# Kernel tuning notes

Hardware: AMD Instinct MI355X
Metric: run time of the kernel (lower is better)

The kernel has to match this reference:

```python
import jax, jax.numpy as jnp
import numpy as np

N = 16384   # total nodes in batch
E = 65536   # edges
B = 512     # sessions
L = 32      # nodes per session
H = 64      # hidden_size
HEADS = 16  # GAT heads (layer 1)
K = 3       # interests
V = 32000   # n_node (item vocab)
NEG = 0.2   # leaky relu slope


def _u(k, shape, stdv):
    return jax.random.uniform(k, shape, jnp.float32, -stdv, stdv)


def setup_inputs():
    key = jax.random.key(0)
    ks = jax.random.split(key, 24)
    s = 1.0 / np.sqrt(H)  # reset_parameters: uniform(-stdv, stdv)
    D = K * H
    return {
        "x": jax.random.randint(ks[0], (N,), 0, V),
        "edge_index": jax.random.randint(ks[1], (2, E), 0, N),
        "batch": jnp.repeat(jnp.arange(B, dtype=jnp.int32), L),
        "embedding": _u(ks[2], (V, H), s),
        "w_interest": _u(ks[3], (H, K), s),
        "gat1_W": _u(ks[4], (K, H, HEADS * H), s),
        "gat1_as": _u(ks[5], (K, HEADS, H), s),
        "gat1_ad": _u(ks[6], (K, HEADS, H), s),
        "gat1_b": _u(ks[7], (K, HEADS * H), s),
        "gat2_W": _u(ks[8], (K, HEADS * H, H), s),
        "gat2_as": _u(ks[9], (K, 1, H), s),
        "gat2_ad": _u(ks[10], (K, 1, H), s),
        "gat2_b": _u(ks[11], (K, H), s),
        "W1_w": _u(ks[12], (D, D), s), "W1_b": _u(ks[13], (D,), s),
        "W2_w": _u(ks[14], (D, D), s), "W2_b": _u(ks[15], (D,), s),
        "q_w": _u(ks[16], (D, 1), s), "q_b": _u(ks[17], (1,), s),
        "W3_w": _u(ks[18], (2 * D, D), s), "W3_b": _u(ks[19], (D,), s),
    }


def _gat(h_in, W, b, a_s, a_d, src, dst, valid, heads, out):
    """PyG GATConv: per-head linear, edge softmax over dest, self-loops for all nodes."""
    n = h_in.shape[0]
    h = (h_in @ W).reshape(n, heads, out)          # [n, heads, out]
    asrc = (h * a_s[None]).sum(-1)                 # [n, heads]
    adst = (h * a_d[None]).sum(-1)
    loop = jnp.arange(n)
    fs = jnp.concatenate([src, loop])              # edges + self-loops
    fd = jnp.concatenate([dst, loop])
    v = jnp.concatenate([valid, jnp.ones((n,), bool)])
    logits = jax.nn.leaky_relu(asrc[fs] + adst[fd], NEG)   # [E+n, heads]
    logits = jnp.where(v[:, None], logits, -1e9)
    m = jax.ops.segment_max(logits, fd, num_segments=n)
    p = jnp.exp(logits - m[fd]) * v[:, None]
    denom = jax.ops.segment_sum(p, fd, num_segments=n)     # [n, heads]
    num = jax.ops.segment_sum(p[:, :, None] * h[fs], fd, num_segments=n)
    return (num / denom[:, :, None]).reshape(n, heads * out) + b


def _model(x, edge_index, batch, embedding, w_interest,
           gat1_W, gat1_as, gat1_ad, gat1_b,
           gat2_W, gat2_as, gat2_ad, gat2_b,
           W1_w, W1_b, W2_w, W2_b, q_w, q_b, W3_w, W3_b):
    e = embedding[x]                                # [N, H]
    g = jax.nn.softmax((e @ w_interest) / 0.1, axis=-1)   # [N, K]
    mask = g > (1.0 / K)                            # interest_mask
    src, dst = edge_index[0], edge_index[1]
    hiddens = []
    for i in range(K):                              # fixed small interest loop
        xi = g[:, i:i + 1] * e                      # einsum('ik,il->ikl')[:, i]
        valid = mask[src, i] & mask[dst, i]         # subgraph edge mask
        h1 = jax.nn.relu(_gat(xi, gat1_W[i], gat1_b[i], gat1_as[i], gat1_ad[i],
                              src, dst, valid, HEADS, H))
        h2 = _gat(h1, gat2_W[i], gat2_b[i], gat2_as[i], gat2_ad[i],
                  src, dst, valid, 1, H)
        hiddens.append(h2)
    sess = jnp.concatenate(hiddens, axis=1)         # [N, K*H]
    # Embedding2Score
    last_idx = jax.ops.segment_max(jnp.arange(N), batch, num_segments=B)
    v_n = sess[last_idx]                            # [B, K*H]  last node per session
    q1 = v_n[batch] @ W1_w + W1_b                   # v_n repeated per node
    q2 = sess @ W2_w + W2_b
    alpha = jax.nn.sigmoid(q1 + q2) @ q_w + q_b     # [N, 1]
    s_g = jax.ops.segment_sum(alpha * sess, batch, num_segments=B)
    s_h = jnp.concatenate([v_n, s_g], axis=1) @ W3_w + W3_b   # [B, K*H]
    s_h = s_h.reshape(B * K, H)                     # multi-interest split
    z = s_h @ embedding.T                           # [B*K, V]
    return z.reshape(B, K, V).max(axis=1)           # [B, V]


def reference(x, edge_index, batch, embedding, w_interest,
              gat1_W, gat1_as, gat1_ad, gat1_b,
              gat2_W, gat2_as, gat2_ad, gat2_b,
              W1_w, W1_b, W2_w, W2_b, q_w, q_b, W3_w, W3_b):
    return _model(x, edge_index, batch, embedding, w_interest,
                  gat1_W, gat1_as, gat1_ad, gat1_b,
                  gat2_W, gat2_as, gat2_ad, gat2_b,
                  W1_w, W1_b, W2_w, W2_b, q_w, q_b, W3_w, W3_b)
```

## Files before the change

kernel.cpp:

```cpp
#include <hip/hip_runtime.h>
#include <math.h>

#define NN 16384
#define EE 65536
#define BB 512
#define VV 32000

typedef unsigned short us_t;
typedef unsigned int u32_t;
typedef __attribute__((ext_vector_type(4))) float f32x4;
typedef __attribute__((ext_vector_type(8))) short bf16x8;
typedef __attribute__((ext_vector_type(4))) unsigned int u32x4;

__device__ __forceinline__ float bf2f(unsigned int u) {
  return __uint_as_float((u & 0xffffu) << 16);
}
__device__ __forceinline__ unsigned short f2bf(float f) {
  unsigned int x = __float_as_uint(f);
  unsigned int r = (x + 0x7fffu + ((x >> 16) & 1u)) >> 16;
  return (unsigned short)r;
}
__device__ __forceinline__ bf16x8 ntld(const us_t* p) {
  return __builtin_nontemporal_load((const bf16x8*)p);
}
__device__ __forceinline__ void ntst(us_t* p, u32_t a, u32_t b, u32_t c, u32_t d) {
  u32x4 v = {a, b, c, d};
  __builtin_nontemporal_store(v, (u32x4*)p);
}
__device__ __forceinline__ float wsum(float v) {
#pragma unroll
  for (int o = 32; o; o >>= 1) v += __shfl_xor(v, o, 64);
  return v;
}
__device__ __forceinline__ float redu16(float v) {
  v += __shfl_xor(v, 1, 64);
  v += __shfl_xor(v, 2, 64);
  v += __shfl_xor(v, 4, 64);
  v += __shfl_xor(v, 8, 64);
  return v;
}
__device__ __forceinline__ float lrelu(float x) { return x > 0.f ? x : 0.2f * x; }

__global__ void k_detect(const void* emb, int* flag) {
  if (threadIdx.x == 0 && blockIdx.x == 0) {
    const us_t* u = (const us_t*)emb;
    int ok = 1;
    for (int i = 0; i < 128; i++) {
      float v = bf2f((unsigned int)u[i]);
      if (!(fabsf(v) <= 0.13f)) { ok = 0; break; }
    }
    *flag = ok;
  }
}

struct PrepArgs {
  const void* src[17];
  void* dst[17];
  int n[17];
  int kind[17];
  int start[18];
};

__global__ void k_prep(PrepArgs pa, const int* __restrict__ flag) {
  int blk = blockIdx.x;
  int s = 0;
  while (s < 16 && blk >= pa.start[s + 1]) s++;
  int i = (blk - pa.start[s]) * 256 + threadIdx.x;
  if (i >= pa.n[s]) return;
  float v = (*flag) ? bf2f((unsigned int)((const us_t*)pa.src[s])[i])
                    : ((const float*)pa.src[s])[i];
  int kind = pa.kind[s];
  if (kind == 0) {
    ((float*)pa.dst[s])[i] = v;
  } else if (kind == 1) {
    ((us_t*)pa.dst[s])[i] = f2bf(v);
  } else if (kind == 2) {
    int ii = i >> 16, r = i & 65535, k = r >> 10, col = r & 1023;
    ((us_t*)pa.dst[s])[(ii << 16) + col * 64 + k] = f2bf(v);
  } else if (kind == 3) {
    int ii = i >> 16, r = i & 65535, k = r >> 6, col = r & 63;
    ((us_t*)pa.dst[s])[(ii << 16) + col * 1024 + k] = f2bf(v);
  } else {
    int k = i / 192, col = i % 192;
    ((us_t*)pa.dst[s])[col * 192 + k] = f2bf(v);
  }
}

__global__ void k_prepWa(const void* __restrict__ g1Wraw,
                         const float* __restrict__ g1as, const float* __restrict__ g1ad,
                         const int* __restrict__ flag, us_t* __restrict__ Waspack) {
  int gid = blockIdx.x * 256 + threadIdx.x;
  if (gid >= 96 * 64) return;
  int c = gid >> 6, k = gid & 63;
  int i = c >> 5, sd = (c >> 4) & 1, h = c & 15;
  const float* av = (sd ? g1ad : g1as) + i * 1024 + h * 64;
  size_t base = (size_t)i * 65536 + (size_t)k * 1024 + h * 64;
  int isbf = *flag;
  float s = 0.f;
  for (int d = 0; d < 64; d++) {
    float wv = isbf ? bf2f((unsigned int)((const us_t*)g1Wraw)[base + d])
                    : ((const float*)g1Wraw)[base + d];
    s += wv * av[d];
  }
  Waspack[c * 64 + k] = f2bf(s);
}

__global__ void k_embed(const int* __restrict__ x, const void* __restrict__ embr,
                        const void* __restrict__ wintr, const int* __restrict__ flag,
                        us_t* __restrict__ e_bf, float* __restrict__ g) {
  int gid = blockIdx.x * blockDim.x + threadIdx.x;
  int n = gid >> 6, lane = gid & 63;
  if (n >= NN) return;
  int isbf = *flag;
  size_t ei = (size_t)x[n] * 64 + lane;
  float v = isbf ? bf2f((unsigned int)((const us_t*)embr)[ei]) : ((const float*)embr)[ei];
  e_bf[(size_t)n * 64 + lane] = f2bf(v);
  float w0, w1, w2;
  if (isbf) {
    const us_t* w = (const us_t*)wintr;
    w0 = bf2f(w[lane * 3 + 0]); w1 = bf2f(w[lane * 3 + 1]); w2 = bf2f(w[lane * 3 + 2]);
  } else {
    const float* w = (const float*)wintr;
    w0 = w[lane * 3 + 0]; w1 = w[lane * 3 + 1]; w2 = w[lane * 3 + 2];
  }
  float t0 = wsum(v * w0), t1 = wsum(v * w1), t2 = wsum(v * w2);
  if (lane == 0) {
    float l0 = t0 / 0.1f, l1 = t1 / 0.1f, l2 = t2 / 0.1f;
    float m = fmaxf(l0, fmaxf(l1, l2));
    float p0 = __expf(l0 - m), p1 = __expf(l1 - m), p2 = __expf(l2 - m);
    float inv = 1.0f / (p0 + p1 + p2);
    g[n * 4 + 0] = p0 * inv; g[n * 4 + 1] = p1 * inv;
    g[n * 4 + 2] = p2 * inv; g[n * 4 + 3] = 0.f;
  }
}

__global__ void k_countv(const int* __restrict__ ei, const float* __restrict__ g,
                         int* __restrict__ countsv) {
  int e = blockIdx.x * 256 + threadIdx.x;
  if (e >= EE) return;
  int s = ei[e], d = ei[EE + e];
  const float thr = 1.0f / 3.0f;
#pragma unroll
  for (int i = 0; i < 3; i++) {
    if (g[s * 4 + i] > thr && g[d * 4 + i] > thr)
      atomicAdd(&countsv[i * NN + d], 1);
  }
}

__global__ void k_scanv(const int* __restrict__ counts, int* __restrict__ offsets) {
  __shared__ int part[256];
  __shared__ int excl[257];
  int t = threadIdx.x;
  int base = t * 192;
  int s = 0;
  for (int j = 0; j < 192; j++) s += counts[base + j];
  part[t] = s;
  __syncthreads();
  if (t == 0) {
    int run = 0;
    for (int j = 0; j < 256; j++) { excl[j] = run; run += part[j]; }
    excl[256] = run;
  }
  __syncthreads();
  int run = excl[t];
  for (int j = 0; j < 192; j++) { offsets[base + j] = run; run += counts[base + j]; }
  if (t == 255) offsets[3 * NN] = excl[256];
}

__global__ void k_fillv(const int* __restrict__ ei, const float* __restrict__ g,
                        const float* __restrict__ eatt,
                        const int* __restrict__ offsetsv, int* __restrict__ fillposv,
                        int2* __restrict__ edgesC, float* __restrict__ easrcP) {
  int e = blockIdx.x * 256 + threadIdx.x;
  if (e >= EE) return;
  int s = ei[e], d = ei[EE + e];
  const float thr = 1.0f / 3.0f;
#pragma unroll
  for (int i = 0; i < 3; i++) {
    float gs = g[s * 4 + i];
    if (gs > thr && g[d * 4 + i] > thr) {
      int pos = offsetsv[i * NN + d] + atomicAdd(&fillposv[i * NN + d], 1);
      edgesC[pos] = make_int2(s, __float_as_int(gs));
      const float* er = &eatt[(size_t)s * 96 + i * 32];
      float* op = &easrcP[(size_t)pos * 16];
#pragma unroll
      for (int h = 0; h < 16; h++) op[h] = gs * er[h];
    }
  }
}

__global__ __launch_bounds__(256) void k_easrc(
    const us_t* __restrict__ e_bf, const us_t* __restrict__ Waspack,
    float* __restrict__ eatt) {
  __shared__ char As[8192];
  int t = threadIdx.x;
  int row0 = blockIdx.x * 64;
  for (int id = t; id < 512; id += 256) {
    int r = id >> 3, c = id & 7;
    uint4 v = *(const uint4*)&e_bf[(size_t)(row0 + r) * 64 + c * 8];
    *(uint4*)(As + r * 128 + ((c ^ (r & 7)) << 4)) = v;
  }
  __syncthreads();
  int wv = t >> 6, L = t & 63, li = L & 15, lq = L >> 4;
#pragma unroll
  for (int ct = 0; ct < 6; ct++) {
    f32x4 acc = {0.f, 0.f, 0.f, 0.f};
#pragma unroll
    for (int ks = 0; ks < 2; ks++) {
      int row = wv * 16 + li;
      bf16x8 af = *(const bf16x8*)(As + row * 128 + (((ks * 4 + lq) ^ (row & 7)) << 4));
      bf16x8 bfr = *(const bf16x8*)(Waspack + (size_t)(ct * 16 + li) * 64 + ks * 32 + lq * 8);
      acc = __builtin_amdgcn_mfma_f32_16x16x32_bf16(af, bfr, acc, 0, 0, 0);
    }
#pragma unroll
    for (int r = 0; r < 4; r++) {
      int row = row0 + wv * 16 + lq * 4 + r;
      eatt[(size_t)row * 96 + ct * 16 + li] = acc[r];
    }
  }
}

__global__ __launch_bounds__(256) void k_phaseA(
    const us_t* __restrict__ e_bf, const float* __restrict__ g,
    const float* __restrict__ eatt,
    const int* __restrict__ offsetsv, const int2* __restrict__ edgesC,
    const float* __restrict__ easrcP, us_t* __restrict__ xagg) {
  int t = threadIdx.x;
  int intr = blockIdx.y;
  int wv = t >> 6, L = t & 63;
  int n = blockIdx.x * 4 + wv;
  int h = L >> 2;
  int doff = (L & 3) * 16;
  float gn = g[n * 4 + intr];
  float ad = gn * eatt[(size_t)n * 96 + intr * 32 + 16 + h];
  float m = lrelu(gn * eatt[(size_t)n * 96 + intr * 32 + h] + ad);
  float den = 1.f;
  float acc[16];
  {
    const uint4* ep = (const uint4*)&e_bf[(size_t)n * 64 + doff];
    uint4 a = ep[0], b = ep[1];
    acc[0] = gn * bf2f(a.x);  acc[1] = gn * bf2f(a.x >> 16);
    acc[2] = gn * bf2f(a.y);  acc[3] = gn * bf2f(a.y >> 16);
    acc[4] = gn * bf2f(a.z);  acc[5] = gn * bf2f(a.z >> 16);
    acc[6] = gn * bf2f(a.w);  acc[7] = gn * bf2f(a.w >> 16);
    acc[8] = gn * bf2f(b.x);  acc[9] = gn * bf2f(b.x >> 16);
    acc[10] = gn * bf2f(b.y); acc[11] = gn * bf2f(b.y >> 16);
    acc[12] = gn * bf2f(b.z); acc[13] = gn * bf2f(b.z >> 16);
    acc[14] = gn * bf2f(b.w); acc[15] = gn * bf2f(b.w >> 16);
  }
  int beg = offsetsv[intr * NN + n], end = offsetsv[intr * NN + n + 1];
  for (int j = beg; j < end; j++) {
    int2 sg = edgesC[j];
    int s = sg.x;
    float gs = __int_as_float(sg.y);
    float l = lrelu(easrcP[(size_t)j * 16 + h] + ad);
    float p = __expf(l - m);
    den += p;
    float pg = p * gs;
    const uint4* ep = (const uint4*)&e_bf[(size_t)s * 64 + doff];
    uint4 a = ep[0], b = ep[1];
    acc[0] += pg * bf2f(a.x);  acc[1] += pg * bf2f(a.x >> 16);
    acc[2] += pg * bf2f(a.y);  acc[3] += pg * bf2f(a.y >> 16);
    acc[4] += pg * bf2f(a.z);  acc[5] += pg * bf2f(a.z >> 16);
    acc[6] += pg * bf2f(a.w);  acc[7] += pg * bf2f(a.w >> 16);
    acc[8] += pg * bf2f(b.x);  acc[9] += pg * bf2f(b.x >> 16);
    acc[10] += pg * bf2f(b.y); acc[11] += pg * bf2f(b.y >> 16);
    acc[12] += pg * bf2f(b.z); acc[13] += pg * bf2f(b.z >> 16);
    acc[14] += pg * bf2f(b.w); acc[15] += pg * bf2f(b.w >> 16);
  }
  float inv = 1.f / den;
  u32_t w[8];
#pragma unroll
  for (int kk = 0; kk < 8; kk++) {
    w[kk] = (u32_t)f2bf(acc[2 * kk] * inv) | ((u32_t)f2bf(acc[2 * kk + 1] * inv) << 16);
  }
  us_t* op = &xagg[(((size_t)intr * 16 + h) * NN + n) * 64 + doff];
  ntst(op, w[0], w[1], w[2], w[3]);
  ntst(op + 8, w[4], w[5], w[6], w[7]);
}

__global__ __launch_bounds__(256) void k_tgemm(
    const us_t* __restrict__ xagg, const us_t* __restrict__ g1Wt,
    const float* __restrict__ b1all, us_t* __restrict__ Tbuf) {
  __shared__ char As[8192];
  __shared__ char Cs[8192];
  int t = threadIdx.x;
  int n0 = blockIdx.x * 64;
  int h = blockIdx.y;
  int intr = blockIdx.z;
  const us_t* xa = xagg + (((size_t)intr * 16 + h) * NN + n0) * 64;
  const us_t* W = g1Wt + (size_t)intr * 65536 + (size_t)(h * 64) * 64;
  const float* b1 = b1all + intr * 1024 + h * 64;
  for (int id = t; id < 512; id += 256) {
    int r = id >> 3, c = id & 7;
    bf16x8 v = ntld(&xa[(size_t)r * 64 + c * 8]);
    *(bf16x8*)(As + r * 128 + ((c ^ (r & 7)) << 4)) = v;
  }
  __syncthreads();
  int wv = t >> 6, L = t & 63, li = L & 15, lq = L >> 4;
  f32x4 acc[4];
#pragma unroll
  for (int ct = 0; ct < 4; ct++) acc[ct] = {0.f, 0.f, 0.f, 0.f};
#pragma unroll
  for (int ks = 0; ks < 2; ks++) {
    int row = wv * 16 + li;
    bf16x8 af = *(const bf16x8*)(As + row * 128 + (((ks * 4 + lq) ^ (row & 7)) << 4));
#pragma unroll
    for (int ct = 0; ct < 4; ct++) {
      bf16x8 bfr = *(const bf16x8*)&W[(size_t)(ct * 16 + li) * 64 + ks * 32 + lq * 8];
      acc[ct] = __builtin_amdgcn_mfma_f32_16x16x32_bf16(af, bfr, acc[ct], 0, 0, 0);
    }
  }
#pragma unroll
  for (int ct = 0; ct < 4; ct++) {
    float bv = b1[ct * 16 + li];
#pragma unroll
    for (int r = 0; r < 4; r++) {
      int row = wv * 16 + lq * 4 + r;
      int byte = (ct * 16 + li) * 2;
      float tv = fmaxf(acc[ct][r] + bv, 0.f);
      *(us_t*)(Cs + row * 128 + (((byte >> 4) ^ (row & 7)) << 4) + (byte & 15)) = f2bf(tv);
    }
  }
  __syncthreads();
  us_t* tb = Tbuf + (((size_t)intr * 16 + h) * NN + n0) * 64;
  for (int id = t; id < 512; id += 256) {
    int r = id >> 3, c = id & 7;
    bf16x8 v = *(const bf16x8*)(Cs + r * 128 + ((c ^ (r & 7)) << 4));
    __builtin_nontemporal_store(v, (bf16x8*)&tb[(size_t)r * 64 + c * 8]);
  }
}

__global__ __launch_bounds__(256) void k_h2gemm(
    const us_t* __restrict__ Tbuf, const us_t* __restrict__ g2Wt,
    const float* __restrict__ g2as, const float* __restrict__ g2ad,
    float* __restrict__ h2pre_a, float* __restrict__ a2s, float* __restrict__ a2d) {
  __shared__ uint4 AsU[1024];
  __shared__ uint4 BsU[1024];
  char* As = (char*)AsU;
  char* Bs = (char*)BsU;
  int t = threadIdx.x;
  int intr = blockIdx.y;
  int row0 = blockIdx.x * 64;
  const us_t* Wt = g2Wt + (size_t)intr * 65536;
  const float* a_s = g2as + intr * 64;
  const float* a_d = g2ad + intr * 64;
  float* h2pre = h2pre_a + (size_t)intr * NN * 64;
  int wv = t >> 6, lane = t & 63, li = lane & 15, lq = lane >> 4;
  f32x4 acc[4];
#pragma unroll
  for (int sub = 0; sub < 4; sub++) acc[sub] = {0.f, 0.f, 0.f, 0.f};
  for (int kb = 0; kb < 8; kb++) {
    __syncthreads();
    for (int id = t; id < 1024; id += 256) {
      int r = id >> 4, c = id & 15;
      int k = kb * 128 + c * 8;
      int h = k >> 6, d = k & 63;
      bf16x8 v = ntld(&Tbuf[(((size_t)intr * 16 + h) * NN + row0 + r) * 64 + d]);
      *(bf16x8*)(As + r * 256 + ((c ^ (r & 15)) << 4)) = v;
      uint4 w = *(const uint4*)&Wt[(size_t)r * 1024 + kb * 128 + c * 8];
      *(uint4*)(Bs + r * 256 + ((c ^ (r & 15)) << 4)) = w;
    }
    __syncthreads();
#pragma unroll
    for (int ks = 0; ks < 4; ks++) {
      int r = wv * 16 + li;
      bf16x8 af = *(const bf16x8*)(As + r * 256 + ((((ks << 2) | lq) ^ (r & 15)) << 4));
#pragma unroll
      for (int sub = 0; sub < 4; sub++) {
        int vr = sub * 16 + li;
        bf16x8 bf_ = *(const bf16x8*)(Bs + vr * 256 + ((((ks << 2) | lq) ^ (vr & 15)) << 4));
        acc[sub] = __builtin_amdgcn_mfma_f32_16x16x32_bf16(af, bf_, acc[sub], 0, 0, 0);
      }
    }
  }
  float asv[4], adv[4];
#pragma unroll
  for (int sub = 0; sub < 4; sub++) {
    asv[sub] = a_s[sub * 16 + li];
    adv[sub] = a_d[sub * 16 + li];
  }
#pragma unroll
  for (int rr = 0; rr < 4; rr++) {
    int n = row0 + wv * 16 + lq * 4 + rr;
    float s = 0.f, d = 0.f;
#pragma unroll
    for (int sub = 0; sub < 4; sub++) {
      float hv = acc[sub][rr];
      h2pre[(size_t)n * 64 + sub * 16 + li] = hv;
      s += hv * asv[sub];
      d += hv * adv[sub];
    }
    s = redu16(s); d = redu16(d);
    if (li == 0) {
      a2s[(size_t)intr * NN + n] = s;
      a2d[(size_t)intr * NN + n] = d;
    }
  }
}

__global__ void k_gat2_agg(const float* __restrict__ h2pre_a,
                           const float* __restrict__ a2s_a, const float* __restrict__ a2d_a,
                           const float* __restrict__ b2all,
                           const int* __restrict__ offsetsv,
                           const int2* __restrict__ edgesC, float* __restrict__ sess) {
  int intr = blockIdx.y;
  int gid = blockIdx.x * blockDim.x + threadIdx.x;
  int n = gid >> 6, lane = gid & 63;
  if (n >= NN) return;
  const float* h2pre = h2pre_a + (size_t)intr * NN * 64;
  const float* a2s = a2s_a + (size_t)intr * NN;
  const float* a2d = a2d_a + (size_t)intr * NN;
  const float* b2 = b2all + intr * 64;
  float ad = a2d[n];
  float m = lrelu(a2s[n] + ad);
  float den = 1.f;
  float acc = h2pre[(size_t)n * 64 + lane];
  int beg = offsetsv[intr * NN + n], end = offsetsv[intr * NN + n + 1];
  for (int j = beg; j < end; j++) {
    int s = edgesC[j].x;
    float l = lrelu(a2s[s] + ad);
    float p = __expf(l - m);
    den += p;
    acc += p * h2pre[(size_t)s * 64 + lane];
  }
  sess[(size_t)n * 192 + intr * 64 + lane] = acc / den + b2[lane];
}

__global__ __launch_bounds__(192) void k_vq1(
    const float* __restrict__ sess,
    const float* __restrict__ W1w, const float* __restrict__ W1b,
    float* __restrict__ vn, float* __restrict__ vq1) {
  __shared__ float row[192];
  int b = blockIdx.x, j = threadIdx.x;
  int li = b * 32 + 31;
  float v = sess[(size_t)li * 192 + j];
  row[j] = v;
  vn[b * 192 + j] = v;
  __syncthreads();
  float acc = W1b[j];
  for (int k = 0; k < 192; k++) acc += row[k] * W1w[k * 192 + j];
  vq1[b * 192 + j] = acc;
}

__global__ __launch_bounds__(256) void k_alpha_sg_mfma(
    const float* __restrict__ sess, const float* __restrict__ vq1,
    const us_t* __restrict__ W2T, const float* __restrict__ W2b,
    const float* __restrict__ qw, const float* __restrict__ qb,
    float* __restrict__ sg) {
  __shared__ char As[64 * 512];
  __shared__ float vq_l[2 * 192];
  __shared__ float w2b_l[192], qw_l[192];
  __shared__ float sg_l[2 * 192];
  int t = threadIdx.x;
  int n0 = blockIdx.x * 64;
  if (t < 192) { w2b_l[t] = W2b[t]; qw_l[t] = qw[t]; }
  for (int id = t; id < 384; id += 256) {
    sg_l[id] = 0.f;
    vq_l[id] = vq1[(size_t)(blockIdx.x * 2) * 192 + id];
  }
  for (int id = t; id < 1536; id += 256) {
    int r = id / 24, c = id % 24;
    const float* p = &sess[(size_t)(n0 + r) * 192 + c * 8];
    float4 f0 = *(const float4*)p;
    float4 f1 = *(const float4*)(p + 4);
    u32_t w0 = (u32_t)f2bf(f0.x) | ((u32_t)f2bf(f0.y) << 16);
    u32_t w1 = (u32_t)f2bf(f0.z) | ((u32_t)f2bf(f0.w) << 16);
    u32_t w2 = (u32_t)f2bf(f1.x) | ((u32_t)f2bf(f1.y) << 16);
    u32_t w3 = (u32_t)f2bf(f1.z) | ((u32_t)f2bf(f1.w) << 16);
    *(uint4*)(As + r * 512 + ((c ^ (r & 7)) << 4)) = make_uint4(w0, w1, w2, w3);
  }
  __syncthreads();
  int wv = t >> 6, lane = t & 63, li = lane & 15, lq = lane >> 4;
  int sl = wv >> 1;
  f32x4 acc[12];
#pragma unroll
  for (int sub = 0; sub < 12; sub++) acc[sub] = {0.f, 0.f, 0.f, 0.f};
#pragma unroll
  for (int ks = 0; ks < 6; ks++) {
    int r = wv * 16 + li;
    bf16x8 af = *(const bf16x8*)(As + r * 512 + (((ks * 4 + lq) ^ (r & 7)) << 4));
#pragma unroll
    for (int sub = 0; sub < 12; sub++) {
      bf16x8 bfr = *(const bf16x8*)&W2T[(size_t)(sub * 16 + li) * 192 + ks * 32 + lq * 8];
      acc[sub] = __builtin_amdgcn_mfma_f32_16x16x32_bf16(af, bfr, acc[sub], 0, 0, 0);
    }
  }
  float qbv = qb[0];
  float s_part[12];
#pragma unroll
  for (int sub = 0; sub < 12; sub++) s_part[sub] = 0.f;
#pragma unroll
  for (int rr = 0; rr < 4; rr++) {
    int n = n0 + wv * 16 + lq * 4 + rr;
    float ap = 0.f;
    float sv[12];
#pragma unroll
    for (int sub = 0; sub < 12; sub++) {
      int col = sub * 16 + li;
      float q = vq_l[sl * 192 + col] + acc[sub][rr] + w2b_l[col];
      float sgm = 1.f / (1.f + __expf(-q));
      ap += sgm * qw_l[col];
      sv[sub] = sess[(size_t)n * 192 + col];
    }
    ap = redu16(ap);
    float alpha = ap + qbv;
#pragma unroll
    for (int sub = 0; sub < 12; sub++) s_part[sub] += alpha * sv[sub];
  }
#pragma unroll
  for (int sub = 0; sub < 12; sub++) {
    float v = s_part[sub];
    v += __shfl_xor(v, 16, 64);
    v += __shfl_xor(v, 32, 64);
    if (lq == 0) atomicAdd(&sg_l[sl * 192 + sub * 16 + li], v);
  }
  __syncthreads();
  for (int id = t; id < 384; id += 256)
    sg[(size_t)(blockIdx.x * 2) * 192 + id] = sg_l[id];
}

__global__ __launch_bounds__(192) void k_sh(
    const float* __restrict__ vn, const float* __restrict__ sg,
    const float* __restrict__ W3w, const float* __restrict__ W3b,
    float* __restrict__ sh) {
  __shared__ float row[384];
  int b = blockIdx.x, j = threadIdx.x;
  row[j] = vn[b * 192 + j];
  row[192 + j] = sg[b * 192 + j];
  __syncthreads();
  float acc = W3b[j];
  for (int k = 0; k < 384; k++) acc += row[k] * W3w[k * 192 + j];
  sh[b * 192 + j] = acc;
}

__global__ __launch_bounds__(256) void k_final_mfma(
    const float* __restrict__ sh, const us_t* __restrict__ emb_bf,
    void* __restrict__ out, const int* __restrict__ flag) {
  __shared__ uint4 AsU[384];
  __shared__ uint4 BsU[2048];
  char* As = (char*)AsU;
  char* Bs = (char*)BsU;
  int t = threadIdx.x;
  int v0 = blockIdx.x * 256, b0 = blockIdx.y * 16;
  for (int id = t; id < 384; id += 256) {
    int i2 = id >> 7, rem = id & 127, r = rem >> 3, c = rem & 7;
    const float* p = &sh[(size_t)(b0 + r) * 192 + i2 * 64 + c * 8];
    float4 f0 = *(const float4*)p;
    float4 f1 = *(const float4*)(p + 4);
    u32_t w0 = (u32_t)f2bf(f0.x) | ((u32_t)f2bf(f0.y) << 16);
    u32_t w1 = (u32_t)f2bf(f0.z) | ((u32_t)f2bf(f0.w) << 16);
    u32_t w2 = (u32_t)f2bf(f1.x) | ((u32_t)f2bf(f1.y) << 16);
    u32_t w3 = (u32_t)f2bf(f1.z) | ((u32_t)f2bf(f1.w) << 16);
    *(uint4*)(As + i2 * 2048 + r * 128 + ((c ^ (r & 7)) << 4)) = make_uint4(w0, w1, w2, w3);
  }
  for (int id = t; id < 2048; id += 256) {
    int vr = id >> 3, c = id & 7;
    uint4 v = *(const uint4*)&emb_bf[(size_t)(v0 + vr) * 64 + c * 8];
    *(uint4*)(Bs + vr * 128 + ((c ^ (vr & 7)) << 4)) = v;
  }
  __syncthreads();
  int wv = t >> 6, lane = t & 63, li = lane & 15, lq = lane >> 4;
  int cb = wv * 64;
  int isbf = *flag;
  f32x4 acc[3][4];
#pragma unroll
  for (int i = 0; i < 3; i++)
#pragma unroll
    for (int sub = 0; sub < 4; sub++) acc[i][sub] = {0.f, 0.f, 0.f, 0.f};
#pragma unroll
  for (int ks = 0; ks < 2; ks++) {
    bf16x8 bfr[4];
#pragma unroll
    for (int sub = 0; sub < 4; sub++) {
      int vr = cb + sub * 16 + li;
      bfr[sub] = *(const bf16x8*)(Bs + vr * 128 + ((((ks << 2) | lq) ^ (vr & 7)) << 4));
    }
#pragma unroll
    for (int i = 0; i < 3; i++) {
      bf16x8 af = *(const bf16x8*)(As + i * 2048 + li * 128 + ((((ks << 2) | lq) ^ (li & 7)) << 4));
#pragma unroll
      for (int sub = 0; sub < 4; sub++)
        acc[i][sub] = __builtin_amdgcn_mfma_f32_16x16x32_bf16(af, bfr[sub], acc[i][sub], 0, 0, 0);
    }
  }
#pragma unroll
  for (int sub = 0; sub < 4; sub++) {
    int col = v0 + cb + sub * 16 + li;
#pragma unroll
    for (int rr = 0; rr < 4; rr++) {
      float o = fmaxf(fmaxf(acc[0][sub][rr], acc[1][sub][rr]), acc[2][sub][rr]);
      int b = b0 + lq * 4 + rr;
      if (isbf) ((us_t*)out)[(size_t)b * VV + col] = f2bf(o);
      else ((float*)out)[(size_t)b * VV + col] = o;
    }
  }
}

extern "C" void kernel_launch(void* const* d_in, const int* in_sizes, int n_in,
                              void* d_out, int out_size, void* d_ws, size_t ws_size,
                              hipStream_t stream) {
  if (n_in < 21) return;
  const int* x = (const int*)d_in[0];
  const int* ei = (const int*)d_in[1];

  char* ws = (char*)d_ws;
  size_t off = 0;
  auto A = [&](size_t bytes) -> char* {
    char* p = ws + off;
    off += (bytes + 255) & ~(size_t)255;
    return p;
  };
  int* flag = (int*)A(4);
  us_t* emb_bf = (us_t*)A((size_t)VV * 64 * 2);
  us_t* e_bf = (us_t*)A((size_t)NN * 64 * 2);
  us_t* g1Wt = (us_t*)A((size_t)3 * 65536 * 2);
  us_t* g2Wt = (us_t*)A((size_t)3 * 65536 * 2);
  us_t* W2T = (us_t*)A((size_t)36864 * 2);
  us_t* Waspack = (us_t*)A((size_t)96 * 64 * 2);
  float* eatt = (float*)A((size_t)NN * 96 * 4);
  float* c_g1as = (float*)A(3072 * 4);
  float* c_g1ad = (float*)A(3072 * 4);
  float* c_g1b = (float*)A(3072 * 4);
  float* c_g2as = (float*)A(192 * 4);
  float* c_g2ad = (float*)A(192 * 4);
  float* c_g2b = (float*)A(192 * 4);
  float* c_W1w = (float*)A(36864 * 4);
  float* c_W1b = (float*)A(192 * 4);
  float* c_W2b = (float*)A(192 * 4);
  float* c_qw = (float*)A(192 * 4);
  float* c_qb = (float*)A(4);
  float* c_W3w = (float*)A(73728 * 4);
  float* c_W3b = (float*)A(192 * 4);
  float* g_buf = (float*)A((size_t)NN * 4 * 4);
  us_t* xagg = (us_t*)A((size_t)3 * NN * 1024 * 2);
  us_t* Tbuf = (us_t*)A((size_t)3 * NN * 1024 * 2);
  float* h2pre = (float*)A((size_t)3 * NN * 64 * 4);
  float* a2s = (float*)A((size_t)3 * NN * 4);
  float* a2d = (float*)A((size_t)3 * NN * 4);
  float* sess = (float*)A((size_t)NN * 192 * 4);
  float* vq1 = (float*)A((size_t)BB * 192 * 4);
  float* sg = (float*)A((size_t)BB * 192 * 4);
  float* vn = (float*)A((size_t)BB * 192 * 4);
  float* shb = (float*)A((size_t)BB * 192 * 4);
  int* countsv = (int*)A((size_t)3 * NN * 4);
  int* offsetsv = (int*)A((size_t)(3 * NN + 1) * 4);
  int* fillposv = (int*)A((size_t)3 * NN * 4);
  int2* edgesC = (int2*)A((size_t)3 * EE * 8);
  float* easrcP = (float*)A((size_t)3 * EE * 16 * 4);
  if (off > ws_size) return;

  hipMemsetAsync(countsv, 0, 3 * NN * 4, stream);
  hipMemsetAsync(fillposv, 0, 3 * NN * 4, stream);

  k_detect<<<1, 64, 0, stream>>>(d_in[3], flag);

  PrepArgs pa;
  int nb = 0, idx = 0;
  auto SEC = [&](const void* s, void* d, int n, int kind) {
    pa.src[idx] = s; pa.dst[idx] = d; pa.n[idx] = n; pa.kind[idx] = kind;
    pa.start[idx] = nb; nb += (n + 255) / 256; idx++;
  };
  SEC(d_in[3], emb_bf, VV * 64, 1);
  SEC(d_in[5], g1Wt, 196608, 2);
  SEC(d_in[9], g2Wt, 196608, 3);
  SEC(d_in[15], W2T, 36864, 4);
  SEC(d_in[6], c_g1as, 3072, 0);
  SEC(d_in[7], c_g1ad, 3072, 0);
  SEC(d_in[8], c_g1b, 3072, 0);
  SEC(d_in[10], c_g2as, 192, 0);
  SEC(d_in[11], c_g2ad, 192, 0);
  SEC(d_in[12], c_g2b, 192, 0);
  SEC(d_in[13], c_W1w, 36864, 0);
  SEC(d_in[14], c_W1b, 192, 0);
  SEC(d_in[16], c_W2b, 192, 0);
  SEC(d_in[17], c_qw, 192, 0);
  SEC(d_in[18], c_qb, 1, 0);
  SEC(d_in[19], c_W3w, 73728, 0);
  SEC(d_in[20], c_W3b, 192, 0);
  pa.start[17] = nb;
  k_prep<<<nb, 256, 0, stream>>>(pa, flag);
  k_prepWa<<<24, 256, 0, stream>>>(d_in[5], c_g1as, c_g1ad, flag, Waspack);

  k_embed<<<NN * 64 / 256, 256, 0, stream>>>(x, d_in[3], d_in[4], flag, e_bf, g_buf);
  k_easrc<<<NN / 64, 256, 0, stream>>>(e_bf, Waspack, eatt);
  k_countv<<<EE / 256, 256, 0, stream>>>(ei, g_buf, countsv);
  k_scanv<<<1, 256, 0, stream>>>(countsv, offsetsv);
  k_fillv<<<EE / 256, 256, 0, stream>>>(ei, g_buf, eatt, offsetsv, fillposv,
                                        edgesC, easrcP);

  k_phaseA<<<dim3(NN / 4, 3), 256, 0, stream>>>(
      e_bf, g_buf, eatt, offsetsv, edgesC, easrcP, xagg);
  k_tgemm<<<dim3(NN / 64, 16, 3), 256, 0, stream>>>(xagg, g1Wt, c_g1b, Tbuf);
  k_h2gemm<<<dim3(NN / 64, 3), 256, 0, stream>>>(
      Tbuf, g2Wt, c_g2as, c_g2ad, h2pre, a2s, a2d);
  k_gat2_agg<<<dim3(NN * 64 / 256, 3), 256, 0, stream>>>(
      h2pre, a2s, a2d, c_g2b, offsetsv, edgesC, sess);

  k_vq1<<<BB, 192, 0, stream>>>(sess, c_W1w, c_W1b, vn, vq1);
  k_alpha_sg_mfma<<<NN / 64, 256, 0, stream>>>(sess, vq1, W2T, c_W2b, c_qw, c_qb, sg);
  k_sh<<<BB, 192, 0, stream>>>(vn, sg, c_W3w, c_W3b, shb);
  k_final_mfma<<<dim3(VV / 256, BB / 16), 256, 0, stream>>>(shb, emb_bf, d_out, flag);
}
```

Measured before the change: 294.6 us.

## Fuse GAT layer-1 head GEMM into layer-2 GEMM, dropping Tbuf round trip

Removes the separate per-head transform kernel and computes relu(xagg·W1+b1) per head tile inside the layer-2 GEMM, keeping the intermediate in LDS. This eliminates writing and re-reading a large bf16 intermediate buffer in global memory and one kernel launch. In exchange the fused kernel has fewer blocks, more LDS per block, and re-reads the layer-1 weights per block from cache.

```diff
diff --git a/kernel.cpp b/kernel.cpp
--- a/kernel.cpp
+++ b/kernel.cpp
@@ -279,93 +279,73 @@
   ntst(op + 8, w[4], w[5], w[6], w[7]);
 }
 
-__global__ __launch_bounds__(256) void k_tgemm(
+__global__ __launch_bounds__(256) void k_h2gemm(
     const us_t* __restrict__ xagg, const us_t* __restrict__ g1Wt,
-    const float* __restrict__ b1all, us_t* __restrict__ Tbuf) {
-  __shared__ char As[8192];
-  __shared__ char Cs[8192];
-  int t = threadIdx.x;
-  int n0 = blockIdx.x * 64;
-  int h = blockIdx.y;
-  int intr = blockIdx.z;
-  const us_t* xa = xagg + (((size_t)intr * 16 + h) * NN + n0) * 64;
-  const us_t* W = g1Wt + (size_t)intr * 65536 + (size_t)(h * 64) * 64;
-  const float* b1 = b1all + intr * 1024 + h * 64;
-  for (int id = t; id < 512; id += 256) {
-    int r = id >> 3, c = id & 7;
-    bf16x8 v = ntld(&xa[(size_t)r * 64 + c * 8]);
-    *(bf16x8*)(As + r * 128 + ((c ^ (r & 7)) << 4)) = v;
-  }
-  __syncthreads();
-  int wv = t >> 6, L = t & 63, li = L & 15, lq = L >> 4;
-  f32x4 acc[4];
-#pragma unroll
-  for (int ct = 0; ct < 4; ct++) acc[ct] = {0.f, 0.f, 0.f, 0.f};
-#pragma unroll
-  for (int ks = 0; ks < 2; ks++) {
-    int row = wv * 16 + li;
-    bf16x8 af = *(const bf16x8*)(As + row * 128 + (((ks * 4 + lq) ^ (row & 7)) << 4));
-#pragma unroll
-    for (int ct = 0; ct < 4; ct++) {
-      bf16x8 bfr = *(const bf16x8*)&W[(size_t)(ct * 16 + li) * 64 + ks * 32 + lq * 8];
-      acc[ct] = __builtin_amdgcn_mfma_f32_16x16x32_bf16(af, bfr, acc[ct], 0, 0, 0);
-    }
-  }
-#pragma unroll
-  for (int ct = 0; ct < 4; ct++) {
-    float bv = b1[ct * 16 + li];
-#pragma unroll
-    for (int r = 0; r < 4; r++) {
-      int row = wv * 16 + lq * 4 + r;
-      int byte = (ct * 16 + li) * 2;
-      float tv = fmaxf(acc[ct][r] + bv, 0.f);
-      *(us_t*)(Cs + row * 128 + (((byte >> 4) ^ (row & 7)) << 4) + (byte & 15)) = f2bf(tv);
-    }
-  }
-  __syncthreads();
-  us_t* tb = Tbuf + (((size_t)intr * 16 + h) * NN + n0) * 64;
-  for (int id = t; id < 512; id += 256) {
-    int r = id >> 3, c = id & 7;
-    bf16x8 v = *(const bf16x8*)(Cs + r * 128 + ((c ^ (r & 7)) << 4));
-    __builtin_nontemporal_store(v, (bf16x8*)&tb[(size_t)r * 64 + c * 8]);
-  }
-}
-
-__global__ __launch_bounds__(256) void k_h2gemm(
-    const us_t* __restrict__ Tbuf, const us_t* __restrict__ g2Wt,
+    const us_t* __restrict__ g2Wt, const float* __restrict__ b1all,
     const float* __restrict__ g2as, const float* __restrict__ g2ad,
     float* __restrict__ h2pre_a, float* __restrict__ a2s, float* __restrict__ a2d) {
-  __shared__ uint4 AsU[1024];
-  __shared__ uint4 BsU[1024];
-  char* As = (char*)AsU;
-  char* Bs = (char*)BsU;
+  __shared__ char As[16384];
+  __shared__ char Bs[16384];
+  __shared__ char Ts[16384];
+  __shared__ float b1s[1024];
   int t = threadIdx.x;
   int intr = blockIdx.y;
   int row0 = blockIdx.x * 64;
-  const us_t* Wt = g2Wt + (size_t)intr * 65536;
+  const us_t* Wt1 = g1Wt + (size_t)intr * 65536;
+  const us_t* Wt2 = g2Wt + (size_t)intr * 65536;
   const float* a_s = g2as + intr * 64;
   const float* a_d = g2ad + intr * 64;
   float* h2pre = h2pre_a + (size_t)intr * NN * 64;
+  for (int id = t; id < 1024; id += 256) b1s[id] = b1all[intr * 1024 + id];
   int wv = t >> 6, lane = t & 63, li = lane & 15, lq = lane >> 4;
   f32x4 acc[4];
 #pragma unroll
   for (int sub = 0; sub < 4; sub++) acc[sub] = {0.f, 0.f, 0.f, 0.f};
   for (int kb = 0; kb < 8; kb++) {
+    int h0 = kb * 2;
     __syncthreads();
     for (int id = t; id < 1024; id += 256) {
       int r = id >> 4, c = id & 15;
-      int k = kb * 128 + c * 8;
-      int h = k >> 6, d = k & 63;
-      bf16x8 v = ntld(&Tbuf[(((size_t)intr * 16 + h) * NN + row0 + r) * 64 + d]);
+      int hh = c >> 3, d = (c & 7) * 8;
+      bf16x8 v = ntld(&xagg[(((size_t)intr * 16 + h0 + hh) * NN + row0 + r) * 64 + d]);
       *(bf16x8*)(As + r * 256 + ((c ^ (r & 15)) << 4)) = v;
-      uint4 w = *(const uint4*)&Wt[(size_t)r * 1024 + kb * 128 + c * 8];
+      uint4 w = *(const uint4*)&Wt2[(size_t)r * 1024 + kb * 128 + c * 8];
       *(uint4*)(Bs + r * 256 + ((c ^ (r & 15)) << 4)) = w;
     }
     __syncthreads();
+#pragma unroll
+    for (int hh = 0; hh < 2; hh++) {
+      int h = h0 + hh;
+      f32x4 c1[4];
+#pragma unroll
+      for (int ct = 0; ct < 4; ct++) c1[ct] = {0.f, 0.f, 0.f, 0.f};
+#pragma unroll
+      for (int ks = 0; ks < 2; ks++) {
+        int r = wv * 16 + li;
+        int ca = hh * 8 + ks * 4 + lq;
+        bf16x8 af = *(const bf16x8*)(As + r * 256 + ((ca ^ (r & 15)) << 4));
+#pragma unroll
+        for (int ct = 0; ct < 4; ct++) {
+          bf16x8 bfr = *(const bf16x8*)&Wt1[(size_t)(h * 64 + ct * 16 + li) * 64 + ks * 32 + lq * 8];
+          c1[ct] = __builtin_amdgcn_mfma_f32_16x16x32_bf16(af, bfr, c1[ct], 0, 0, 0);
+        }
+      }
+#pragma unroll
+      for (int ct = 0; ct < 4; ct++) {
+        float bv = b1s[h * 64 + ct * 16 + li];
+#pragma unroll
+        for (int r = 0; r < 4; r++) {
+          int row = wv * 16 + lq * 4 + r;
+          int byte = (hh * 64 + ct * 16 + li) * 2;
+          float tv = fmaxf(c1[ct][r] + bv, 0.f);
+          *(us_t*)(Ts + row * 256 + (((byte >> 4) ^ (row & 15)) << 4) + (byte & 15)) = f2bf(tv);
+        }
+      }
+    }
 #pragma unroll
     for (int ks = 0; ks < 4; ks++) {
       int r = wv * 16 + li;
-      bf16x8 af = *(const bf16x8*)(As + r * 256 + ((((ks << 2) | lq) ^ (r & 15)) << 4));
+      bf16x8 af = *(const bf16x8*)(Ts + r * 256 + ((((ks << 2) | lq) ^ (r & 15)) << 4));
 #pragma unroll
       for (int sub = 0; sub < 4; sub++) {
         int vr = sub * 16 + li;
@@ -634,7 +614,6 @@
   float* c_W3b = (float*)A(192 * 4);
   float* g_buf = (float*)A((size_t)NN * 4 * 4);
   us_t* xagg = (us_t*)A((size_t)3 * NN * 1024 * 2);
-  us_t* Tbuf = (us_t*)A((size_t)3 * NN * 1024 * 2);
   float* h2pre = (float*)A((size_t)3 * NN * 64 * 4);
   float* a2s = (float*)A((size_t)3 * NN * 4);
   float* a2d = (float*)A((size_t)3 * NN * 4);
@@ -691,9 +670,8 @@
 
   k_phaseA<<<dim3(NN / 4, 3), 256, 0, stream>>>(
       e_bf, g_buf, eatt, offsetsv, edgesC, easrcP, xagg);
-  k_tgemm<<<dim3(NN / 64, 16, 3), 256, 0, stream>>>(xagg, g1Wt, c_g1b, Tbuf);
   k_h2gemm<<<dim3(NN / 64, 3), 256, 0, stream>>>(
-      Tbuf, g2Wt, c_g2as, c_g2ad, h2pre, a2s, a2d);
+      xagg, g1Wt, g2Wt, c_g1b, c_g2as, c_g2ad, h2pre, a2s, a2d);
   k_gat2_agg<<<dim3(NN * 64 / 256, 3), 256, 0, stream>>>(
       h2pre, a2s, a2d, c_g2b, offsetsv, edgesC, sess);
 
```

Result: faster. 268.0 us, median of 3 (-9.0%).
